# Kernel tuning notes

Hardware: AMD Instinct MI355X
Metric: run time of the kernel (lower is better)

Reference implementation:

```python
import jax, jax.numpy as jnp
import numpy as np

NUM_HEADS = 16
EMB = 1024
V_IN = 512
V_OUT = 1024


def setup_inputs() -> dict:
    key = jax.random.key(0)
    ks = jax.random.split(key, 11)
    s = 0.02
    return {
        "query": jax.random.normal(ks[0], (8, 512, EMB), jnp.float32),
        "key": jax.random.normal(ks[1], (8, 1024, V_IN), jnp.float32),
        "value": jax.random.normal(ks[2], (8, 1024, V_IN), jnp.float32),
        "Wq": jax.random.normal(ks[3], (EMB, EMB), jnp.float32) * s,
        "bq": jax.random.normal(ks[4], (EMB,), jnp.float32) * s,
        "Wk": jax.random.normal(ks[5], (V_IN, EMB), jnp.float32) * s,
        "bk": jax.random.normal(ks[6], (EMB,), jnp.float32) * s,
        "Wv": jax.random.normal(ks[7], (V_IN, V_OUT), jnp.float32) * s,
        "bv": jax.random.normal(ks[8], (V_OUT,), jnp.float32) * s,
        "Wo": jax.random.normal(ks[9], (V_OUT, EMB), jnp.float32) * s,
        "bo": jax.random.normal(ks[10], (EMB,), jnp.float32) * s,
    }


def reference(query, key, value, Wq, bq, Wk, bk, Wv, bv, Wo, bo):
    B, Lq, _ = query.shape
    Lk = key.shape[1]
    H = NUM_HEADS
    dh = EMB // H          # 64, key/query head dim (used as softmax scale)
    dv = V_OUT // H        # 64, value head dim
    q = (query @ Wq + bq).reshape(B, Lq, H, dh)   # [B,Lq,H,dh]
    k = (key @ Wk + bk).reshape(B, Lk, H, dh)     # [B,Lk,H,dh]
    v = (value @ Wv + bv).reshape(B, Lk, H, dv)   # [B,Lk,H,dv]
    scale = 1.0 / np.sqrt(dh).astype(np.float32)
    scores = jnp.einsum('bqhd,bkhd->bhqk', q * scale, k)  # [B,H,Lq,Lk]
    attn = jax.nn.softmax(scores, axis=-1)
    ctx = jnp.einsum('bhqk,bkhd->bqhd', attn, v).reshape(B, Lq, V_OUT)
    return ctx @ Wo + bo  # [B,Lq,EMB]
```

## Files before the change

kernel.cpp:

```cpp
#include <hip/hip_runtime.h>
#include <hip/hip_bf16.h>

#define EMB  1024
#define VIN  512
#define VOUT 1024
#define NH   16
#define DH   64
#define BB   8
#define LQ   512
#define LK   1024

typedef __attribute__((ext_vector_type(8))) short bf16x8;
typedef __attribute__((ext_vector_type(4))) float f32x4;

typedef const __attribute__((address_space(1))) unsigned int* gptr_t;
typedef __attribute__((address_space(3))) unsigned int* lptr_t;

__device__ __forceinline__ unsigned short f2bf(float x) {
    unsigned int u = __float_as_uint(x);
    u += 0x7FFF + ((u >> 16) & 1);
    return (unsigned short)(u >> 16);
}
__device__ __forceinline__ float bf2f(unsigned short h) {
    return __uint_as_float(((unsigned int)h) << 16);
}
__device__ __forceinline__ float fexp2(float x) {
    return __builtin_amdgcn_exp2f(x);
}
__device__ __forceinline__ unsigned int pk2bf(float a, float b) {
    float2 f; f.x = a; f.y = b;
    __hip_bfloat162 t = __float22bfloat162_rn(f);
    return *reinterpret_cast<unsigned int*>(&t);
}

#define SWZ(row, cb) (((row) << 7) + ((cb) ^ (((row) & 7) << 4)))

__device__ __forceinline__ void wtile(const float* W, unsigned short* Wht,
                                      unsigned short* Wlt, int K, int N,
                                      int bx, int by, int tx, int ty)
{
    __shared__ float t[32][33];
    const int n0 = bx * 32, k0 = by * 32;
#pragma unroll
    for (int r = 0; r < 32; r += 8)
        t[ty + r][tx] = W[(size_t)(k0 + ty + r) * N + n0 + tx];
    __syncthreads();
#pragma unroll
    for (int r = 0; r < 32; r += 8) {
        float x = t[tx][ty + r];
        unsigned short h = f2bf(x);
        size_t o = (size_t)(n0 + ty + r) * K + k0 + tx;
        Wht[o] = h;
        if (Wlt) Wlt[o] = f2bf(x - bf2f(h));
    }
}

__global__ __launch_bounds__(256) void convert_all(const float* __restrict__ q,
                                                   const float* __restrict__ k,
                                                   const float* __restrict__ v,
                                                   const float* __restrict__ Wq,
                                                   const float* __restrict__ Wk,
                                                   const float* __restrict__ Wv,
                                                   const float* __restrict__ Wo,
                                                   unsigned short* __restrict__ Aq,
                                                   unsigned short* __restrict__ Ak,
                                                   unsigned short* __restrict__ Av,
                                                   unsigned short* __restrict__ Wqt,
                                                   unsigned short* __restrict__ Wkt,
                                                   unsigned short* __restrict__ Wvt,
                                                   unsigned short* __restrict__ Woh,
                                                   unsigned short* __restrict__ Wol)
{
    const int id = blockIdx.x;
    if (id < 12288) {
        const int which = id >> 12;
        const float* in = (which == 0) ? q : (which == 1) ? k : v;
        unsigned short* out = (which == 0) ? Aq : (which == 1) ? Ak : Av;
        const int i = (id & 4095) * 256 + threadIdx.x;
        float val[4];
        *reinterpret_cast<float4*>(val) = *reinterpret_cast<const float4*>(&in[(size_t)i * 4]);
        unsigned short h[4];
#pragma unroll
        for (int j = 0; j < 4; ++j) h[j] = f2bf(val[j]);
        *reinterpret_cast<uint2*>(&out[(size_t)i * 4]) = *reinterpret_cast<uint2*>(h);
    } else {
        const int wid = id - 12288;
        const int tx = threadIdx.x & 31, ty = threadIdx.x >> 5;
        if (wid < 1024)      wtile(Wq, Wqt, nullptr, 1024, 1024, wid & 31, wid >> 5, tx, ty);
        else if (wid < 1536) wtile(Wk, Wkt, nullptr, 512, 1024, (wid - 1024) & 31, (wid - 1024) >> 5, tx, ty);
        else if (wid < 2048) wtile(Wv, Wvt, nullptr, 512, 1024, (wid - 1536) & 31, (wid - 1536) >> 5, tx, ty);
        else                 wtile(Wo, Woh, Wol, 1024, 1024, (wid - 2048) & 31, (wid - 2048) >> 5, tx, ty);
    }
}

__device__ __forceinline__ void stagehalf(const unsigned short* g0, int Kstride,
                                          unsigned short* l0, int lane)
{
#pragma unroll
    for (int r = 0; r < 8; ++r) {
        int row  = r * 8 + (lane >> 3);
        int colb = ((lane & 7) << 4) ^ ((row & 7) << 4);
        const unsigned short* src = g0 + (size_t)row * Kstride + (colb >> 1);
        __builtin_amdgcn_global_load_lds((gptr_t)src, (lptr_t)(l0 + r * 512), 16, 0, 0);
    }
}

__global__ __launch_bounds__(256, 2) void gemm_qkv(const unsigned short* __restrict__ Aq,
                                                   const unsigned short* __restrict__ Ak,
                                                   const unsigned short* __restrict__ Av,
                                                   const unsigned short* __restrict__ Wqt,
                                                   const unsigned short* __restrict__ Wkt,
                                                   const unsigned short* __restrict__ Wvt,
                                                   const float* __restrict__ bq,
                                                   const float* __restrict__ bk,
                                                   const float* __restrict__ bv,
                                                   unsigned short* __restrict__ Qh,
                                                   unsigned short* __restrict__ Kh,
                                                   unsigned short* __restrict__ Vth)
{
    __shared__ unsigned short As[2][128 * 64], Bs[2][128 * 64];

    const int id  = blockIdx.x;
    const int seg = (id < 256) ? 0 : (id < 768) ? 1 : 2;
    const int lid = id - ((seg == 0) ? 0 : (seg == 1) ? 256 : 768);
    const int nwg = (seg == 0) ? 256 : 512;
    const int K   = (seg == 0) ? 1024 : 512;
    const unsigned short* Ah  = (seg == 0) ? Aq : (seg == 1) ? Ak : Av;
    const unsigned short* Bht = (seg == 0) ? Wqt : (seg == 1) ? Wkt : Wvt;
    const float* bias = (seg == 0) ? bq : (seg == 1) ? bk : bv;
    unsigned short* Ch = (seg == 0) ? Qh : (seg == 1) ? Kh : Vth;
    const int N = 1024;

    const int qq  = nwg >> 3;
    const int swz = (lid & 7) * qq + (lid >> 3);
    const int bx = swz & 7, by = swz >> 3;
    const int m0 = by * 128, n0 = bx * 128;

    const int tid  = threadIdx.x;
    const int lane = tid & 63;
    const int w    = tid >> 6;
    const int wm = (w & 1) * 64;
    const int wn = (w >> 1) * 64;
    const int lr = lane & 15;
    const int lk = lane >> 4;

    f32x4 acc[4][4];
#pragma unroll
    for (int i = 0; i < 4; ++i)
#pragma unroll
        for (int j = 0; j < 4; ++j) acc[i][j] = (f32x4)(0.f);

    const unsigned short* mysrc = (w < 2)
        ? Ah  + (size_t)(m0 + (w & 1) * 64) * K
        : Bht + (size_t)(n0 + (w & 1) * 64) * K;
    const int lofs = (w & 1) * 4096;
    unsigned short* pl0 = ((w < 2) ? As[0] : Bs[0]) + lofs;
    unsigned short* pl1 = ((w < 2) ? As[1] : Bs[1]) + lofs;

    stagehalf(mysrc, K, pl0, lane);

    const int nt = K >> 6;
    for (int t = 0; t < nt; ++t) {
        __syncthreads();
        if (t + 1 < nt)
            stagehalf(mysrc + ((size_t)(t + 1) << 6), K, ((t & 1) ? pl0 : pl1), lane);

        const char* Ac = (const char*)As[t & 1];
        const char* Bc = (const char*)Bs[t & 1];
#pragma unroll
        for (int ks = 0; ks < 2; ++ks) {
            bf16x8 ah[4], bh[4];
            const int cb = ks * 64 + lk * 16;
#pragma unroll
            for (int f = 0; f < 4; ++f) {
                ah[f] = *reinterpret_cast<const bf16x8*>(Ac + SWZ(wm + f * 16 + lr, cb));
                bh[f] = *reinterpret_cast<const bf16x8*>(Bc + SWZ(wn + f * 16 + lr, cb));
            }
#pragma unroll
            for (int fm = 0; fm < 4; ++fm)
#pragma unroll
                for (int fn = 0; fn < 4; ++fn)
                    acc[fm][fn] = __builtin_amdgcn_mfma_f32_16x16x32_bf16(ah[fm], bh[fn], acc[fm][fn], 0, 0, 0);
        }
    }

#pragma unroll
    for (int fn = 0; fn < 4; ++fn) {
        const int col = n0 + wn + fn * 16 + lr;
        const float bv_ = bias[col];
#pragma unroll
        for (int fm = 0; fm < 4; ++fm) {
            const int row0 = m0 + wm + fm * 16 + lk * 4;
            if (seg == 0) {
#pragma unroll
                for (int r = 0; r < 4; ++r)
                    Ch[(size_t)(row0 + r) * N + col] = f2bf((acc[fm][fn][r] + bv_) * 0.18033688011112042f);
            } else if (seg == 1) {
#pragma unroll
                for (int r = 0; r < 4; ++r)
                    Ch[(size_t)(row0 + r) * N + col] = f2bf(acc[fm][fn][r] + bv_);
            } else {
                unsigned short h4[4];
#pragma unroll
                for (int r = 0; r < 4; ++r)
                    h4[r] = f2bf(acc[fm][fn][r] + bv_);
                size_t o = (((size_t)((row0 >> 10) * NH + (col >> 6)) * 64 + (col & 63)) << 10) + (row0 & 1023);
                *reinterpret_cast<uint2*>(&Ch[o]) = *reinterpret_cast<uint2*>(h4);
            }
        }
    }
}

__device__ __forceinline__ void stageplane(const unsigned short* g0, int Kstride,
                                           unsigned short* l0, int lane)
{
#pragma unroll
    for (int r = 0; r < 16; ++r) {
        int row  = r * 8 + (lane >> 3);
        int colb = ((lane & 7) << 4) ^ ((row & 7) << 4);
        const unsigned short* src = g0 + (size_t)row * Kstride + (colb >> 1);
        __builtin_amdgcn_global_load_lds((gptr_t)src, (lptr_t)(l0 + r * 512), 16, 0, 0);
    }
}

__global__ __launch_bounds__(256) void gemm2(const unsigned short* __restrict__ Ah,
                                             const unsigned short* __restrict__ Al,
                                             const unsigned short* __restrict__ Bht,
                                             const unsigned short* __restrict__ Blt,
                                             const float* __restrict__ bias,
                                             float* __restrict__ C,
                                             int M, int N, int K)
{
    __shared__ unsigned short As_h[2][128 * 64], As_l[2][128 * 64];
    __shared__ unsigned short Bs_h[2][128 * 64], Bs_l[2][128 * 64];

    const int nbx = N >> 7;
    const int nwg = gridDim.x;
    const int qq  = nwg >> 3;
    const int id  = blockIdx.x;
    const int swz = (id & 7) * qq + (id >> 3);
    const int bx = swz % nbx, by = swz / nbx;
    const int m0 = by * 128, n0 = bx * 128;

    const int tid  = threadIdx.x;
    const int lane = tid & 63;
    const int w    = tid >> 6;
    const int wm = (w & 1) * 64;
    const int wn = (w >> 1) * 64;
    const int lr = lane & 15;
    const int lk = lane >> 4;

    f32x4 acc[4][4];
#pragma unroll
    for (int i = 0; i < 4; ++i)
#pragma unroll
        for (int j = 0; j < 4; ++j) acc[i][j] = (f32x4)(0.f);

    const unsigned short* mysrc =
        (w == 0) ? Ah + (size_t)m0 * K :
        (w == 1) ? Al + (size_t)m0 * K :
        (w == 2) ? Bht + (size_t)n0 * K :
                   Blt + (size_t)n0 * K;
    unsigned short* pl0 = (w == 0) ? As_h[0] : (w == 1) ? As_l[0] : (w == 2) ? Bs_h[0] : Bs_l[0];
    unsigned short* pl1 = (w == 0) ? As_h[1] : (w == 1) ? As_l[1] : (w == 2) ? Bs_h[1] : Bs_l[1];

    stageplane(mysrc, K, pl0, lane);

    const int nt = K >> 6;
    for (int t = 0; t < nt; ++t) {
        __syncthreads();
        if (t + 1 < nt)
            stageplane(mysrc + ((size_t)(t + 1) << 6), K, ((t & 1) ? pl0 : pl1), lane);

        const char* Ahc = (const char*)As_h[t & 1];
        const char* Alc = (const char*)As_l[t & 1];
        const char* Bhc = (const char*)Bs_h[t & 1];
        const char* Blc = (const char*)Bs_l[t & 1];
#pragma unroll
        for (int ks = 0; ks < 2; ++ks) {
            bf16x8 ah[4], al[4], bh[4], bl[4];
            const int cb = ks * 64 + lk * 16;
#pragma unroll
            for (int f = 0; f < 4; ++f) {
                int rowA = wm + f * 16 + lr;
                ah[f] = *reinterpret_cast<const bf16x8*>(Ahc + SWZ(rowA, cb));
                al[f] = *reinterpret_cast<const bf16x8*>(Alc + SWZ(rowA, cb));
                int rowB = wn + f * 16 + lr;
                bh[f] = *reinterpret_cast<const bf16x8*>(Bhc + SWZ(rowB, cb));
                bl[f] = *reinterpret_cast<const bf16x8*>(Blc + SWZ(rowB, cb));
            }
#pragma unroll
            for (int fm = 0; fm < 4; ++fm)
#pragma unroll
                for (int fn = 0; fn < 4; ++fn) {
                    acc[fm][fn] = __builtin_amdgcn_mfma_f32_16x16x32_bf16(ah[fm], bh[fn], acc[fm][fn], 0, 0, 0);
                    acc[fm][fn] = __builtin_amdgcn_mfma_f32_16x16x32_bf16(ah[fm], bl[fn], acc[fm][fn], 0, 0, 0);
                    acc[fm][fn] = __builtin_amdgcn_mfma_f32_16x16x32_bf16(al[fm], bh[fn], acc[fm][fn], 0, 0, 0);
                }
        }
    }

#pragma unroll
    for (int fn = 0; fn < 4; ++fn) {
        const int col = n0 + wn + fn * 16 + lr;
        const float bv = bias[col];
#pragma unroll
        for (int fm = 0; fm < 4; ++fm) {
            const int row0 = m0 + wm + fm * 16 + lk * 4;
#pragma unroll
            for (int r = 0; r < 4; ++r)
                C[(size_t)(row0 + r) * N + col] = acc[fm][fn][r] + bv;
        }
    }
}

__device__ __forceinline__ void stage32(const unsigned short* g0, unsigned short* l0, int lane)
{
#pragma unroll
    for (int r = 0; r < 4; ++r) {
        int row  = r * 8 + (lane >> 3);
        int colb = ((lane & 7) << 4) ^ ((row & 7) << 4);
        const unsigned short* src = g0 + ((size_t)row << 10) + (colb >> 1);
        __builtin_amdgcn_global_load_lds((gptr_t)src, (lptr_t)(l0 + r * 512), 16, 0, 0);
    }
}

__global__ __launch_bounds__(256, 4) void attn_mfma(const unsigned short* __restrict__ Qh,
                                                    const unsigned short* __restrict__ Kh,
                                                    const unsigned short* __restrict__ Vth,
                                                    unsigned short* __restrict__ Ch,
                                                    unsigned short* __restrict__ Cl)
{
    const int id  = blockIdx.x;
    const int qt  = (id >> 3) & 7;
    const int grp = (id & 7) | ((id >> 6) << 3);
    const int h = grp & 15, b = grp >> 4;

    const int tid  = threadIdx.x;
    const int lane = tid & 63;
    const int w    = tid >> 6;
    const int lr   = lane & 15;
    const int lk   = lane >> 4;

    __shared__ unsigned short KVs[2][2][4096];
    __shared__ unsigned short Ps[4][1024];

    bf16x8 qb[2];
    {
        const unsigned short* qrow = &Qh[(size_t)(b * LQ + qt * 64 + w * 16 + lr) * EMB + h * DH];
        qb[0] = *reinterpret_cast<const bf16x8*>(qrow + lk * 8);
        qb[1] = *reinterpret_cast<const bf16x8*>(qrow + 32 + lk * 8);
    }

    const unsigned short* K0 = Kh + ((size_t)(b * LK) << 10) + h * DH;
    const unsigned short* V0 = Vth + ((size_t)(grp * 64) << 10);

    {
        const int half = (w & 1) * 32;
        if (w < 2) stage32(K0 + ((size_t)half << 10), KVs[0][0] + half * 64, lane);
        else       stage32(V0 + ((size_t)half << 10), KVs[0][1] + half * 64, lane);
    }

    float m = -1e30f, lsum = 0.f;
    f32x4 acc[4];
#pragma unroll
    for (int f = 0; f < 4; ++f) acc[f] = (f32x4)(0.f);

    for (int kt = 0; kt < LK / 64; ++kt) {
        const int cur = kt & 1;
        __syncthreads();

        if (kt + 1 < LK / 64) {
            const size_t koff = (size_t)(kt + 1) * 64;
            const int half = (w & 1) * 32;
            if (w < 2) stage32(K0 + ((koff + half) << 10), KVs[cur ^ 1][0] + half * 64, lane);
            else       stage32(V0 + ((size_t)half << 10) + koff, KVs[cur ^ 1][1] + half * 64, lane);
        }

        const char* Ks = (const char*)KVs[cur][0];
        const char* Vs = (const char*)KVs[cur][1];

        f32x4 s[4];
#pragma unroll
        for (int fn = 0; fn < 4; ++fn) s[fn] = (f32x4)(0.f);
        __builtin_amdgcn_s_setprio(1);
#pragma unroll
        for (int ks = 0; ks < 2; ++ks) {
            const int cb = ks * 64 + lk * 16;
#pragma unroll
            for (int fn = 0; fn < 4; ++fn) {
                bf16x8 kb = *reinterpret_cast<const bf16x8*>(Ks + SWZ(fn * 16 + lr, cb));
                s[fn] = __builtin_amdgcn_mfma_f32_16x16x32_bf16(kb, qb[ks], s[fn], 0, 0, 0);
            }
        }
        __builtin_amdgcn_s_setprio(0);

        {
            f32x4 t4 = s[0];
#pragma unroll
            for (int fn = 1; fn < 4; ++fn)
#pragma unroll
                for (int r = 0; r < 4; ++r) t4[r] = fmaxf(t4[r], s[fn][r]);
            float lmx = fmaxf(fmaxf(t4[0], t4[1]), fmaxf(t4[2], t4[3]));

            if (!__all(lmx <= m + 8.f)) {
                float mx = fmaxf(lmx, __shfl_xor(lmx, 16));
                mx = fmaxf(mx, __shfl_xor(mx, 32));
                float mnew = fmaxf(m, mx);
                float corr = fexp2(m - mnew);
                m = mnew;
                lsum *= corr;
#pragma unroll
                for (int f = 0; f < 4; ++f)
#pragma unroll
                    for (int r = 0; r < 4; ++r) acc[f][r] *= corr;
            }
            float rs = 0.f;
#pragma unroll
            for (int fn = 0; fn < 4; ++fn)
#pragma unroll
                for (int r = 0; r < 4; ++r) {
                    float p = fexp2(s[fn][r] - m);
                    s[fn][r] = p;
                    rs += p;
                }
            rs += __shfl_xor(rs, 16);
            rs += __shfl_xor(rs, 32);
            lsum += rs;
        }

#pragma unroll
        for (int fn = 0; fn < 4; ++fn) {
            uint2 pk;
            pk.x = pk2bf(s[fn][0], s[fn][1]);
            pk.y = pk2bf(s[fn][2], s[fn][3]);
            *reinterpret_cast<uint2*>((char*)Ps[w] + SWZ(lr, fn * 32 + lk * 8)) = pk;
        }

        __builtin_amdgcn_s_setprio(1);
#pragma unroll
        for (int ks = 0; ks < 2; ++ks) {
            const int cb = ks * 64 + lk * 16;
            bf16x8 pa = *reinterpret_cast<const bf16x8*>((char*)Ps[w] + SWZ(lr, cb));
#pragma unroll
            for (int f = 0; f < 4; ++f) {
                bf16x8 vb = *reinterpret_cast<const bf16x8*>(Vs + SWZ(f * 16 + lr, cb));
                acc[f] = __builtin_amdgcn_mfma_f32_16x16x32_bf16(vb, pa, acc[f], 0, 0, 0);
            }
        }
        __builtin_amdgcn_s_setprio(0);
    }

    {
        float inv = 1.f / lsum;
        const size_t row = (size_t)(b * LQ + qt * 64 + w * 16 + lr);
#pragma unroll
        for (int f = 0; f < 4; ++f)
#pragma unroll
            for (int r = 0; r < 4; ++r) {
                float x = acc[f][r] * inv;
                unsigned short hh = f2bf(x);
                size_t o = (row << 10) + h * DH + f * 16 + lk * 4 + r;
                Ch[o] = hh;
                Cl[o] = f2bf(x - bf2f(hh));
            }
    }
}

extern "C" void kernel_launch(void* const* d_in, const int* in_sizes, int n_in,
                              void* d_out, int out_size, void* d_ws, size_t ws_size,
                              hipStream_t stream)
{
    const float* query = (const float*)d_in[0];
    const float* key   = (const float*)d_in[1];
    const float* value = (const float*)d_in[2];
    const float* Wq = (const float*)d_in[3];
    const float* bq = (const float*)d_in[4];
    const float* Wk = (const float*)d_in[5];
    const float* bk = (const float*)d_in[6];
    const float* Wv = (const float*)d_in[7];
    const float* bv = (const float*)d_in[8];
    const float* Wo = (const float*)d_in[9];
    const float* bo = (const float*)d_in[10];
    float* out = (float*)d_out;

    unsigned short* Qh  = (unsigned short*)d_ws;
    unsigned short* Kh  = Qh  + (size_t)4194304;
    unsigned short* Vth = Kh  + (size_t)8388608;
    unsigned short* Aq  = Vth + (size_t)8388608;
    unsigned short* Ak  = Aq  + (size_t)4194304;
    unsigned short* Av  = Ak  + (size_t)4194304;
    unsigned short* Ch  = Av  + (size_t)4194304;
    unsigned short* Cl  = Ch  + (size_t)4194304;
    unsigned short* Wqt = Cl  + (size_t)4194304;
    unsigned short* Wkt = Wqt + (size_t)1048576;
    unsigned short* Wvt = Wkt + (size_t)524288;
    unsigned short* Woh = Wvt + (size_t)524288;
    unsigned short* Wol = Woh + (size_t)1048576;

    convert_all<<<15360, 256, 0, stream>>>(query, key, value, Wq, Wk, Wv, Wo,
                                           Aq, Ak, Av, Wqt, Wkt, Wvt, Woh, Wol);
    gemm_qkv<<<1280, 256, 0, stream>>>(Aq, Ak, Av, Wqt, Wkt, Wvt, bq, bk, bv, Qh, Kh, Vth);

    attn_mfma<<<LQ / 64 * NH * BB, 256, 0, stream>>>(Qh, Kh, Vth, Ch, Cl);

    gemm2<<<(EMB / 128) * (BB * LQ / 128), 256, 0, stream>>>(Ch, Cl, Woh, Wol, bo, out, BB * LQ, EMB, VOUT);
}
```

Before: 122.2 us.

## Fuse fp32-to-bf16 activation conversion into QKV GEMM staging and vectorize context stores

The separate conversion pass over query/key/value is removed. The QKV GEMM now loads fp32 activations directly, converts them to bf16 in registers and writes them swizzled into LDS, which avoids writing and re-reading a bf16 copy of the activations through global memory. The cost is that A-tile staging becomes synchronous register loads instead of async global_load_lds, so global latency is less hidden, and fp32 reads double the bytes per A tile. The attention epilogue also packs four bf16 hi/lo values into 8-byte stores instead of scalar 2-byte stores.

```diff
diff --git a/kernel.cpp b/kernel.cpp
--- a/kernel.cpp
+++ b/kernel.cpp
@@ -55,42 +55,22 @@
     }
 }
 
-__global__ __launch_bounds__(256) void convert_all(const float* __restrict__ q,
-                                                   const float* __restrict__ k,
-                                                   const float* __restrict__ v,
-                                                   const float* __restrict__ Wq,
-                                                   const float* __restrict__ Wk,
-                                                   const float* __restrict__ Wv,
-                                                   const float* __restrict__ Wo,
-                                                   unsigned short* __restrict__ Aq,
-                                                   unsigned short* __restrict__ Ak,
-                                                   unsigned short* __restrict__ Av,
-                                                   unsigned short* __restrict__ Wqt,
-                                                   unsigned short* __restrict__ Wkt,
-                                                   unsigned short* __restrict__ Wvt,
-                                                   unsigned short* __restrict__ Woh,
-                                                   unsigned short* __restrict__ Wol)
-{
-    const int id = blockIdx.x;
-    if (id < 12288) {
-        const int which = id >> 12;
-        const float* in = (which == 0) ? q : (which == 1) ? k : v;
-        unsigned short* out = (which == 0) ? Aq : (which == 1) ? Ak : Av;
-        const int i = (id & 4095) * 256 + threadIdx.x;
-        float val[4];
-        *reinterpret_cast<float4*>(val) = *reinterpret_cast<const float4*>(&in[(size_t)i * 4]);
-        unsigned short h[4];
-#pragma unroll
-        for (int j = 0; j < 4; ++j) h[j] = f2bf(val[j]);
-        *reinterpret_cast<uint2*>(&out[(size_t)i * 4]) = *reinterpret_cast<uint2*>(h);
-    } else {
-        const int wid = id - 12288;
-        const int tx = threadIdx.x & 31, ty = threadIdx.x >> 5;
-        if (wid < 1024)      wtile(Wq, Wqt, nullptr, 1024, 1024, wid & 31, wid >> 5, tx, ty);
-        else if (wid < 1536) wtile(Wk, Wkt, nullptr, 512, 1024, (wid - 1024) & 31, (wid - 1024) >> 5, tx, ty);
-        else if (wid < 2048) wtile(Wv, Wvt, nullptr, 512, 1024, (wid - 1536) & 31, (wid - 1536) >> 5, tx, ty);
-        else                 wtile(Wo, Woh, Wol, 1024, 1024, (wid - 2048) & 31, (wid - 2048) >> 5, tx, ty);
-    }
+__global__ __launch_bounds__(256) void wconvert(const float* __restrict__ Wq,
+                                                const float* __restrict__ Wk,
+                                                const float* __restrict__ Wv,
+                                                const float* __restrict__ Wo,
+                                                unsigned short* __restrict__ Wqt,
+                                                unsigned short* __restrict__ Wkt,
+                                                unsigned short* __restrict__ Wvt,
+                                                unsigned short* __restrict__ Woh,
+                                                unsigned short* __restrict__ Wol)
+{
+    const int wid = blockIdx.x;
+    const int tx = threadIdx.x & 31, ty = threadIdx.x >> 5;
+    if (wid < 1024)      wtile(Wq, Wqt, nullptr, 1024, 1024, wid & 31, wid >> 5, tx, ty);
+    else if (wid < 1536) wtile(Wk, Wkt, nullptr, 512, 1024, (wid - 1024) & 31, (wid - 1024) >> 5, tx, ty);
+    else if (wid < 2048) wtile(Wv, Wvt, nullptr, 512, 1024, (wid - 1536) & 31, (wid - 1536) >> 5, tx, ty);
+    else                 wtile(Wo, Woh, Wol, 1024, 1024, (wid - 2048) & 31, (wid - 2048) >> 5, tx, ty);
 }
 
 __device__ __forceinline__ void stagehalf(const unsigned short* g0, int Kstride,
@@ -105,9 +85,28 @@
     }
 }
 
-__global__ __launch_bounds__(256, 2) void gemm_qkv(const unsigned short* __restrict__ Aq,
-                                                   const unsigned short* __restrict__ Ak,
-                                                   const unsigned short* __restrict__ Av,
+__device__ __forceinline__ void stagehalfA(const float* g0, int Kstride,
+                                           unsigned short* l0, int lane)
+{
+#pragma unroll
+    for (int i = 0; i < 16; ++i) {
+        int flat = i * 64 + lane;
+        int row  = flat >> 4;
+        int c8   = flat & 15;
+        float v[4];
+        *reinterpret_cast<float4*>(v) =
+            *reinterpret_cast<const float4*>(&g0[(size_t)row * Kstride + c8 * 4]);
+        unsigned short h[4];
+#pragma unroll
+        for (int j = 0; j < 4; ++j) h[j] = f2bf(v[j]);
+        int off = (row << 7) + ((c8 * 8) ^ ((row & 7) << 4));
+        *reinterpret_cast<uint2*>((char*)l0 + off) = *reinterpret_cast<uint2*>(h);
+    }
+}
+
+__global__ __launch_bounds__(256, 2) void gemm_qkv(const float* __restrict__ qin,
+                                                   const float* __restrict__ kin,
+                                                   const float* __restrict__ vin,
                                                    const unsigned short* __restrict__ Wqt,
                                                    const unsigned short* __restrict__ Wkt,
                                                    const unsigned short* __restrict__ Wvt,
@@ -125,7 +124,7 @@
     const int lid = id - ((seg == 0) ? 0 : (seg == 1) ? 256 : 768);
     const int nwg = (seg == 0) ? 256 : 512;
     const int K   = (seg == 0) ? 1024 : 512;
-    const unsigned short* Ah  = (seg == 0) ? Aq : (seg == 1) ? Ak : Av;
+    const float* Af = (seg == 0) ? qin : (seg == 1) ? kin : vin;
     const unsigned short* Bht = (seg == 0) ? Wqt : (seg == 1) ? Wkt : Wvt;
     const float* bias = (seg == 0) ? bq : (seg == 1) ? bk : bv;
     unsigned short* Ch = (seg == 0) ? Qh : (seg == 1) ? Kh : Vth;
@@ -150,20 +149,24 @@
 #pragma unroll
         for (int j = 0; j < 4; ++j) acc[i][j] = (f32x4)(0.f);
 
-    const unsigned short* mysrc = (w < 2)
-        ? Ah  + (size_t)(m0 + (w & 1) * 64) * K
-        : Bht + (size_t)(n0 + (w & 1) * 64) * K;
+    const float* asrc = Af + (size_t)(m0 + (w & 1) * 64) * K;
+    const unsigned short* bsrc = Bht + (size_t)(n0 + (w & 1) * 64) * K;
     const int lofs = (w & 1) * 4096;
-    unsigned short* pl0 = ((w < 2) ? As[0] : Bs[0]) + lofs;
-    unsigned short* pl1 = ((w < 2) ? As[1] : Bs[1]) + lofs;
-
-    stagehalf(mysrc, K, pl0, lane);
+    unsigned short* apl0 = As[0] + lofs;
+    unsigned short* apl1 = As[1] + lofs;
+    unsigned short* bpl0 = Bs[0] + lofs;
+    unsigned short* bpl1 = Bs[1] + lofs;
+
+    if (w < 2) stagehalfA(asrc, K, apl0, lane);
+    else       stagehalf(bsrc, K, bpl0, lane);
 
     const int nt = K >> 6;
     for (int t = 0; t < nt; ++t) {
         __syncthreads();
-        if (t + 1 < nt)
-            stagehalf(mysrc + ((size_t)(t + 1) << 6), K, ((t & 1) ? pl0 : pl1), lane);
+        if (t + 1 < nt) {
+            if (w < 2) stagehalfA(asrc + ((t + 1) << 6), K, ((t & 1) ? apl0 : apl1), lane);
+            else       stagehalf(bsrc + ((size_t)(t + 1) << 6), K, ((t & 1) ? bpl0 : bpl1), lane);
+        }
 
         const char* Ac = (const char*)As[t & 1];
         const char* Bc = (const char*)Bs[t & 1];
@@ -455,15 +458,18 @@
         float inv = 1.f / lsum;
         const size_t row = (size_t)(b * LQ + qt * 64 + w * 16 + lr);
 #pragma unroll
-        for (int f = 0; f < 4; ++f)
+        for (int f = 0; f < 4; ++f) {
+            unsigned short h4[4], l4[4];
 #pragma unroll
             for (int r = 0; r < 4; ++r) {
                 float x = acc[f][r] * inv;
-                unsigned short hh = f2bf(x);
-                size_t o = (row << 10) + h * DH + f * 16 + lk * 4 + r;
-                Ch[o] = hh;
-                Cl[o] = f2bf(x - bf2f(hh));
-            }
+                h4[r] = f2bf(x);
+                l4[r] = f2bf(x - bf2f(h4[r]));
+            }
+            size_t o = (row << 10) + h * DH + f * 16 + lk * 4;
+            *reinterpret_cast<uint2*>(&Ch[o]) = *reinterpret_cast<uint2*>(h4);
+            *reinterpret_cast<uint2*>(&Cl[o]) = *reinterpret_cast<uint2*>(l4);
+        }
     }
 }
 
@@ -487,10 +493,7 @@
     unsigned short* Qh  = (unsigned short*)d_ws;
     unsigned short* Kh  = Qh  + (size_t)4194304;
     unsigned short* Vth = Kh  + (size_t)8388608;
-    unsigned short* Aq  = Vth + (size_t)8388608;
-    unsigned short* Ak  = Aq  + (size_t)4194304;
-    unsigned short* Av  = Ak  + (size_t)4194304;
-    unsigned short* Ch  = Av  + (size_t)4194304;
+    unsigned short* Ch  = Vth + (size_t)8388608;
     unsigned short* Cl  = Ch  + (size_t)4194304;
     unsigned short* Wqt = Cl  + (size_t)4194304;
     unsigned short* Wkt = Wqt + (size_t)1048576;
@@ -498,9 +501,8 @@
     unsigned short* Woh = Wvt + (size_t)524288;
     unsigned short* Wol = Woh + (size_t)1048576;
 
-    convert_all<<<15360, 256, 0, stream>>>(query, key, value, Wq, Wk, Wv, Wo,
-                                           Aq, Ak, Av, Wqt, Wkt, Wvt, Woh, Wol);
-    gemm_qkv<<<1280, 256, 0, stream>>>(Aq, Ak, Av, Wqt, Wkt, Wvt, bq, bk, bv, Qh, Kh, Vth);
+    wconvert<<<3072, 256, 0, stream>>>(Wq, Wk, Wv, Wo, Wqt, Wkt, Wvt, Woh, Wol);
+    gemm_qkv<<<1280, 256, 0, stream>>>(query, key, value, Wqt, Wkt, Wvt, bq, bk, bv, Qh, Kh, Vth);
 
     attn_mfma<<<LQ / 64 * NH * BB, 256, 0, stream>>>(Qh, Kh, Vth, Ch, Cl);
 
```

Result: slower. 132.4 us (+8.4%).
